# Optimization experiments

Measured on AMD Instinct MI355X. Metric: run time of the kernel, lower is better.

The kernel has to match this reference:

```python
import jax, jax.numpy as jnp
import numpy as np

B, N, D_IN, D_HID, D_OUT = 64, 512, 512, 512, 512


def setup_inputs() -> dict:
    key = jax.random.key(0)
    ks = jax.random.split(key, 8)
    gain = 0.02  # xavier_normal_ gain used in reset_parameters_xavier

    def xavier(k, fan_in, fan_out):
        std = gain * np.sqrt(2.0 / (fan_in + fan_out))
        return jax.random.normal(k, (fan_in, fan_out), dtype=jnp.float32) * std

    return {
        "batch_graph": jax.random.normal(ks[0], (B, N, D_IN), dtype=jnp.float32),
        "adj": jax.random.uniform(ks[1], (B, N, N), dtype=jnp.float32),
        "W1": xavier(ks[2], D_IN, D_HID),
        "b1": jnp.zeros((D_HID,), dtype=jnp.float32),
        "W2": xavier(ks[3], D_HID, D_HID),
        "b2": jnp.zeros((D_HID,), dtype=jnp.float32),
        "W3": xavier(ks[4], D_HID, D_OUT),
        "b3": jnp.zeros((D_OUT,), dtype=jnp.float32),
    }


def _normalize_adj(adj):
    # rowsum^-0.5 with inf -> 0 (original: torch.pow then isinf mask)
    rowsum = adj.sum(axis=1)                       # [B, N] (sum over dim 1, as in torch)
    safe = jnp.where(rowsum == 0, 1.0, rowsum)
    r = jnp.where(rowsum == 0, 0.0, safe ** -0.5)  # [B, N]
    # (adj @ D)^T @ D = D @ adj^T @ D with D = diag(r)
    return r[:, :, None] * jnp.swapaxes(adj, 1, 2) * r[:, None, :]


def reference(batch_graph, adj, W1, b1, W2, b2, W3, b3):
    # Block-diagonal big_adj @ big_graph == per-graph batched matmul.
    A = _normalize_adj(adj)  # [B, N, N]

    def gc(x, W, b):
        # support = x @ W ; output = A @ support + b
        return jnp.einsum('bij,bjd->bid', A, x @ W) + b

    # dropout is identity in eval mode (deterministic reference)
    x = jax.nn.relu(gc(batch_graph, W1, b1))
    x = jax.nn.relu(gc(x, W2, b2))
    return gc(x, W3, b3)  # [B, N, D_OUT]
```

## Files before the change

kernel.cpp:

```cpp
#include <hip/hip_runtime.h>
#include <cstdint>
#include <cstddef>

typedef _Float16 f16;
typedef _Float16 f16x4 __attribute__((ext_vector_type(4)));
typedef _Float16 f16x8 __attribute__((ext_vector_type(8)));
typedef float    f32x4 __attribute__((ext_vector_type(4)));

#define NB 64
#define NN 262144

__device__ __forceinline__ void gload_lds16(const void* g, void* l) {
    __builtin_amdgcn_global_load_lds(
        (const __attribute__((address_space(1))) void*)g,
        (__attribute__((address_space(3))) void*)l, 16, 0, 0);
}

__device__ __forceinline__ int SWC(int row, int col) {
    return ((((col >> 2) ^ (row >> 2)) & 15) << 2) | (col & 3);
}

__global__ __launch_bounds__(256)
void k_prep(const float* __restrict__ adj, f16* __restrict__ A_raw,
            float* __restrict__ part,
            const float* __restrict__ W1, const float* __restrict__ W2,
            const float* __restrict__ W3, f16* __restrict__ Wt,
            const float* __restrict__ X0, f16* __restrict__ Xa) {
    __shared__ __align__(16) float t[4096];
    __shared__ float red[4][64];
    const int bid = blockIdx.x, tid = threadIdx.x;

    bool do_cvt = false;
    int cvt_idx = 0;
    if (bid < 8192) {
        if (bid & 1) { do_cvt = true; cvt_idx = bid >> 1; }
    } else if (bid < 12288) {
        do_cvt = true; cvt_idx = 4096 + (bid - 8192);
    }

    if (do_cvt) {
        size_t i = ((size_t)cvt_idx * 256 + tid) * 8;
        float4 v0 = *(const float4*)(X0 + i);
        float4 v1 = *(const float4*)(X0 + i + 4);
        f16x8 o;
        o[0] = (f16)v0.x; o[1] = (f16)v0.y; o[2] = (f16)v0.z; o[3] = (f16)v0.w;
        o[4] = (f16)v1.x; o[5] = (f16)v1.y; o[6] = (f16)v1.z; o[7] = (f16)v1.w;
        *(f16x8*)(Xa + i) = o;
    } else if (bid < 8192) {
        const int idx = bid >> 1;
        const int xcd = idx & 7, loc = idx >> 3;
        const int b = xcd * 8 + (loc >> 6);
        const int tile = loc & 63;
        const int i0 = (tile >> 3) * 64, j0 = (tile & 7) * 64;
        const int jt = tile & 7;
        const float* ab = adj + (size_t)b * NN;
        #pragma unroll
        for (int s = 0; s < 4; ++s) {
            int rr = s * 16 + (tid >> 4);
            int creal = SWC(rr, (tid & 15) * 4);
            gload_lds16(&ab[(size_t)(j0 + rr) * 512 + i0 + creal],
                        &t[s * 1024 + tid * 4]);
        }
        asm volatile("s_waitcnt vmcnt(0)" ::: "memory");
        __syncthreads();
        {
            int c = tid & 63, g = tid >> 6;
            float sg = 0.f;
            #pragma unroll
            for (int s = 0; s < 16; ++s) {
                int row = g * 16 + s;
                sg += t[row * 64 + SWC(row, c)];
            }
            red[g][c] = sg;
        }
        f16* Ab = A_raw + (size_t)b * NN;
        int jq = (tid & 15) * 4;
        int ib = tid >> 4;
        #pragma unroll
        for (int s = 0; s < 4; ++s) {
            int ii = ib + s * 16;
            f16x4 o;
            #pragma unroll
            for (int q = 0; q < 4; ++q)
                o[q] = (f16)t[(jq + q) * 64 + SWC(jq + q, ii)];
            *(f16x4*)&Ab[(size_t)(i0 + ii) * 512 + j0 + jq] = o;
        }
        __syncthreads();
        if (tid < 64)
            part[((size_t)b * 8 + jt) * 512 + i0 + tid] =
                red[0][tid] + red[1][tid] + red[2][tid] + red[3][tid];
    } else {
        int cb = bid - 12288;
        int z = cb >> 6, rem = cb & 63;
        const float* W = z == 0 ? W1 : (z == 1 ? W2 : W3);
        f16* out = Wt + (size_t)z * NN;
        int k0 = (rem >> 3) * 64, d0 = (rem & 7) * 64;
        int c = tid & 63, r4 = tid >> 6;
        #pragma unroll
        for (int s = 0; s < 16; ++s) {
            int rr = r4 + s * 4;
            t[rr * 64 + SWC(rr, c)] = W[(size_t)(k0 + rr) * 512 + d0 + c];
        }
        __syncthreads();
        int kq = (tid & 15) * 4;
        int db = tid >> 4;
        #pragma unroll
        for (int s = 0; s < 4; ++s) {
            int dd = db + s * 16;
            f16x4 o;
            #pragma unroll
            for (int q = 0; q < 4; ++q)
                o[q] = (f16)(64.f * t[(kq + q) * 64 + SWC(kq + q, dd)]);
            *(f16x4*)&out[(size_t)(d0 + dd) * 512 + k0 + kq] = o;
        }
    }
}

template<bool BIAS, bool RELU, bool OUTF32, bool RM, bool RN>
__global__ __launch_bounds__(512, 1)
void gemm8(const f16* __restrict__ P, size_t pstr,
           const f16* __restrict__ Qt, size_t qstr,
           void* __restrict__ Cout, size_t cstr,
           const float* __restrict__ bias, const float* __restrict__ part,
           float iscale, float oscale) {
    __shared__ __align__(16) f16 Albuf[2][16384];
    __shared__ __align__(16) f16 Blbuf[2][16384];
    __shared__ float rs_lds[256];

    const int tid  = threadIdx.x;
    const int lane = tid & 63;
    const int wid  = tid >> 6;
    const int wm   = wid >> 2;
    const int wn   = wid & 3;

    const int wg  = blockIdx.x;
    const int swz = (wg & 7) * 32 + (wg >> 3);
    const int b   = swz >> 2;
    const int tt  = swz & 3;
    const int m0  = (tt >> 1) * 256;
    const int n0  = (tt & 1) * 256;

    const f16* Pb = P + (size_t)b * pstr;
    const f16* Qb = Qt + (size_t)b * qstr;

    const int fr = lane & 15, fs = lane >> 4, fx = fr & 7;

    if ((RM || RN) && tid < 256) {
        const float* p = part + (size_t)b * 4096 + (RM ? m0 : n0) + tid;
        float s = 0.f;
        #pragma unroll
        for (int jt = 0; jt < 8; ++jt) s += p[jt * 512];
        rs_lds[tid] = (s > 0.f) ? rsqrtf(s) : 0.f;
    }
    asm volatile("s_waitcnt vmcnt(0)" ::: "memory");

    auto stage_half = [&](const f16* __restrict__ Gb, int row0g, f16* buf, int h, int k0) {
        {
            int row = tid >> 3, sl = tid & 7;
            gload_lds16(Gb + (size_t)(row0g + h * 128 + row) * 512 + k0 + ((sl ^ (row & 7)) * 8),
                        buf + h * 8192 + tid * 8);
        }
        {
            int u = tid + 512;
            int row = u >> 3, sl = u & 7;
            gload_lds16(Gb + (size_t)(row0g + h * 128 + row) * 512 + k0 + ((sl ^ (row & 7)) * 8),
                        buf + h * 8192 + u * 8);
        }
    };

    f32x4 acc[8][4] = {};
    f16x8 af[4][2], bf[2][2];

    stage_half(Qb, n0, &Blbuf[0][0], 0, 0);
    stage_half(Qb, n0, &Blbuf[0][0], 1, 0);
    stage_half(Pb, m0, &Albuf[0][0], 0, 0);
    stage_half(Pb, m0, &Albuf[0][0], 1, 0);

#define LOAD_AF(QM)                                                            \
    _Pragma("unroll") for (int i = 0; i < 4; ++i) {                            \
        int row = wm * 128 + ((QM) * 4 + i) * 16 + fr;                         \
        _Pragma("unroll") for (int k = 0; k < 2; ++k)                          \
            af[i][k] = *(const f16x8*)&Al[row * 64 + ((fs + 4 * k) ^ fx) * 8]; \
    }
#define LOAD_BF(QN)                                                            \
    _Pragma("unroll") for (int j = 0; j < 2; ++j) {                            \
        int row = wn * 64 + ((QN) * 2 + j) * 16 + fr;                          \
        _Pragma("unroll") for (int k = 0; k < 2; ++k)                          \
            bf[j][k] = *(const f16x8*)&Bl[row * 64 + ((fs + 4 * k) ^ fx) * 8]; \
    }
#define PH_SYNC()                                                              \
    __builtin_amdgcn_s_barrier();                                              \
    asm volatile("s_waitcnt lgkmcnt(0)" ::: "memory");                         \
    __builtin_amdgcn_sched_barrier(0);
#define DO_MFMA(QM, QN)                                                        \
    __builtin_amdgcn_s_setprio(1);                                             \
    _Pragma("unroll") for (int i = 0; i < 4; ++i)                              \
        _Pragma("unroll") for (int j = 0; j < 2; ++j)                          \
            _Pragma("unroll") for (int k = 0; k < 2; ++k)                      \
                acc[(QM) * 4 + i][(QN) * 2 + j] =                              \
                    __builtin_amdgcn_mfma_f32_16x16x32_f16(                    \
                        af[i][k], bf[j][k], acc[(QM) * 4 + i][(QN) * 2 + j],   \
                        0, 0, 0);                                              \
    __builtin_amdgcn_s_setprio(0);                                             \
    __builtin_amdgcn_s_barrier();

    for (int t = 0; t < 8; ++t) {
        f16* Al = &Albuf[t & 1][0];
        f16* Bl = &Blbuf[t & 1][0];
        f16* An = &Albuf[(t & 1) ^ 1][0];
        f16* Bn = &Blbuf[(t & 1) ^ 1][0];
        const int kn = (t + 1) * 64;

        asm volatile("s_waitcnt vmcnt(0)" ::: "memory");
        __builtin_amdgcn_s_barrier();

        LOAD_AF(0) LOAD_BF(0)
        if (t < 7) stage_half(Qb, n0, Bn, 0, kn);
        PH_SYNC(); DO_MFMA(0, 0)
        LOAD_BF(1)
        if (t < 7) stage_half(Qb, n0, Bn, 1, kn);
        PH_SYNC(); DO_MFMA(0, 1)
        LOAD_AF(1)
        if (t < 7) stage_half(Pb, m0, An, 0, kn);
        PH_SYNC(); DO_MFMA(1, 1)
        LOAD_BF(0)
        if (t < 7) stage_half(Pb, m0, An, 1, kn);
        PH_SYNC(); DO_MFMA(1, 0)
    }
#undef LOAD_AF
#undef LOAD_BF
#undef PH_SYNC
#undef DO_MFMA

    const int cmb = (lane >> 4) * 4;
    f32x4 rm4[8];
    float rn1[4];
    if (RM) {
        #pragma unroll
        for (int mi = 0; mi < 8; ++mi)
            rm4[mi] = *(const f32x4*)&rs_lds[wm * 128 + mi * 16 + cmb];
    }
    if (RN) {
        #pragma unroll
        for (int ni = 0; ni < 4; ++ni)
            rn1[ni] = rs_lds[wn * 64 + ni * 16 + fr];
    }
    #pragma unroll
    for (int mi = 0; mi < 8; ++mi) {
        #pragma unroll
        for (int ni = 0; ni < 4; ++ni) {
            const int n = n0 + wn * 64 + ni * 16 + fr;
            const int m = m0 + wm * 128 + mi * 16 + cmb;
            float v[4];
            #pragma unroll
            for (int q = 0; q < 4; ++q) {
                float x = acc[mi][ni][q] * iscale;
                if (RM) x *= rm4[mi][q];
                if (RN) x *= rn1[ni];
                if (BIAS) x += bias[m + q];
                if (RELU) x = fmaxf(x, 0.f);
                v[q] = x * oscale;
            }
            if (OUTF32) {
                float* Cb = (float*)Cout + (size_t)b * cstr;
                f32x4 o; o[0] = v[0]; o[1] = v[1]; o[2] = v[2]; o[3] = v[3];
                *(f32x4*)&Cb[(size_t)n * 512 + m] = o;
            } else {
                f16* Cb = (f16*)Cout + (size_t)b * cstr;
                f16x4 o; o[0] = (f16)v[0]; o[1] = (f16)v[1]; o[2] = (f16)v[2]; o[3] = (f16)v[3];
                *(f16x4*)&Cb[(size_t)n * 512 + m] = o;
            }
        }
    }
}

extern "C" void kernel_launch(void* const* d_in, const int* in_sizes, int n_in,
                              void* d_out, int out_size, void* d_ws, size_t ws_size,
                              hipStream_t stream) {
    const float* X0  = (const float*)d_in[0];
    const float* adj = (const float*)d_in[1];
    const float* W1  = (const float*)d_in[2];
    const float* b1  = (const float*)d_in[3];
    const float* W2  = (const float*)d_in[4];
    const float* b2  = (const float*)d_in[5];
    const float* W3  = (const float*)d_in[6];
    const float* b3  = (const float*)d_in[7];

    uint8_t* ws = (uint8_t*)d_ws;
    float* part = (float*)ws;
    f16* Wt1 = (f16*)(ws + (1 << 20));
    f16* A_raw = (f16*)(ws + (1 << 20) + (size_t)3 * NN * 2);
    f16* Xa  = A_raw + (size_t)NB * NN;
    f16* S_t = Xa + (size_t)NB * NN;

    k_prep<<<dim3(12480), dim3(256), 0, stream>>>(adj, A_raw, part, W1, W2, W3, Wt1, X0, Xa);

    dim3 gg(256), gb(512);
    gemm8<false, false, false, true,  false><<<gg, gb, 0, stream>>>(Xa,  (size_t)NN, Wt1, (size_t)0,  S_t, (size_t)NN, nullptr, part, 4.f, 1.f);
    gemm8<true,  true,  false, false, true ><<<gg, gb, 0, stream>>>(S_t, (size_t)NN, A_raw, (size_t)NN, Xa, (size_t)NN, b1, part, 1.f / 256.f, 256.f);
    gemm8<false, false, false, true,  false><<<gg, gb, 0, stream>>>(Xa,  (size_t)NN, Wt1 + NN, (size_t)0,  S_t, (size_t)NN, nullptr, part, 16.f, 1.f);
    gemm8<true,  true,  false, false, true ><<<gg, gb, 0, stream>>>(S_t, (size_t)NN, A_raw, (size_t)NN, Xa, (size_t)NN, b2, part, 1.f / 262144.f, 256.f);
    gemm8<false, false, false, true,  false><<<gg, gb, 0, stream>>>(Xa,  (size_t)NN, Wt1 + 2 * NN, (size_t)0,  S_t, (size_t)NN, nullptr, part, 16.f, 1.f);
    gemm8<true,  false, true,  false, true ><<<gg, gb, 0, stream>>>(S_t, (size_t)NN, A_raw, (size_t)NN, d_out, (size_t)NN, b3, part, 1.f / 262144.f, 1.f);
}
```

Measured before the change: 200.9 us.

## Make prep kernel persistent with double-buffered async LDS staging

The prep kernel's grid shrinks from thousands of single-tile blocks to about 2k blocks. Each block loops over several conversion chunks or transpose tiles and prefetches the next chunk into a second LDS buffer while processing the current one. X conversion now also goes through LDS via async global-to-LDS loads, and the W transpose shares the adj tile path with a scale factor. The intent is to hide memory latency and cut block launch overhead. The risk is fewer resident waves for latency hiding and extra barriers per iteration.

```diff
diff --git a/kernel.cpp b/kernel.cpp
--- a/kernel.cpp
+++ b/kernel.cpp
@@ -26,44 +26,92 @@
             const float* __restrict__ W1, const float* __restrict__ W2,
             const float* __restrict__ W3, f16* __restrict__ Wt,
             const float* __restrict__ X0, f16* __restrict__ Xa) {
-    __shared__ __align__(16) float t[4096];
+    __shared__ __align__(16) float tb[2][4096];
     __shared__ float red[4][64];
     const int bid = blockIdx.x, tid = threadIdx.x;
 
-    bool do_cvt = false;
-    int cvt_idx = 0;
-    if (bid < 8192) {
-        if (bid & 1) { do_cvt = true; cvt_idx = bid >> 1; }
-    } else if (bid < 12288) {
-        do_cvt = true; cvt_idx = 4096 + (bid - 8192);
-    }
-
-    if (do_cvt) {
-        size_t i = ((size_t)cvt_idx * 256 + tid) * 8;
-        float4 v0 = *(const float4*)(X0 + i);
-        float4 v1 = *(const float4*)(X0 + i + 4);
-        f16x8 o;
-        o[0] = (f16)v0.x; o[1] = (f16)v0.y; o[2] = (f16)v0.z; o[3] = (f16)v0.w;
-        o[4] = (f16)v1.x; o[5] = (f16)v1.y; o[6] = (f16)v1.z; o[7] = (f16)v1.w;
-        *(f16x8*)(Xa + i) = o;
-    } else if (bid < 8192) {
-        const int idx = bid >> 1;
-        const int xcd = idx & 7, loc = idx >> 3;
-        const int b = xcd * 8 + (loc >> 6);
-        const int tile = loc & 63;
-        const int i0 = (tile >> 3) * 64, j0 = (tile & 7) * 64;
-        const int jt = tile & 7;
-        const float* ab = adj + (size_t)b * NN;
+    const bool is_cvt = (bid < 2048) && (bid & 1);
+    if (is_cvt) {
+        const int cw = bid >> 1;
+        auto stage_u = [&](int k, int buf) {
+            const float* src = X0 + (size_t)(cw * 8 + k) * 2048;
+            gload_lds16(src + tid * 4,          &tb[buf][tid * 4]);
+            gload_lds16(src + (tid + 256) * 4,  &tb[buf][(tid + 256) * 4]);
+        };
+        stage_u(0, 0);
+        #pragma unroll 1
+        for (int k = 0; k < 8; ++k) {
+            const int buf = k & 1;
+            if (k < 7) {
+                stage_u(k + 1, buf ^ 1);
+                asm volatile("s_waitcnt vmcnt(2)" ::: "memory");
+            } else {
+                asm volatile("s_waitcnt vmcnt(0)" ::: "memory");
+            }
+            __builtin_amdgcn_s_barrier();
+            f32x4 v0 = *(const f32x4*)&tb[buf][tid * 8];
+            f32x4 v1 = *(const f32x4*)&tb[buf][tid * 8 + 4];
+            f16x8 o;
+            o[0] = (f16)v0[0]; o[1] = (f16)v0[1]; o[2] = (f16)v0[2]; o[3] = (f16)v0[3];
+            o[4] = (f16)v1[0]; o[5] = (f16)v1[1]; o[6] = (f16)v1[2]; o[7] = (f16)v1[3];
+            *(f16x8*)(Xa + (size_t)(cw * 8 + k) * 2048 + tid * 8) = o;
+            asm volatile("s_waitcnt lgkmcnt(0)" ::: "memory");
+            __builtin_amdgcn_s_barrier();
+        }
+        return;
+    }
+
+    const int tw = (bid < 2048) ? (bid >> 1) : (bid - 1024);
+    auto decode = [&](int jj, const float*& src, f16*& dst, float& scale,
+                      float*& pp) {
+        int job = tw * 4 + jj;
+        if (job < 4096) {
+            int xcd = job & 7, loc = job >> 3;
+            int b = xcd * 8 + (loc >> 6);
+            int tile = loc & 63;
+            int i0 = (tile >> 3) * 64, j0 = (tile & 7) * 64;
+            src = adj + (size_t)b * NN + (size_t)j0 * 512 + i0;
+            dst = A_raw + (size_t)b * NN + (size_t)i0 * 512 + j0;
+            scale = 1.f;
+            pp = part + ((size_t)b * 8 + (tile & 7)) * 512 + i0;
+        } else {
+            int w = job - 4096;
+            int z = w >> 6, rem = w & 63;
+            int k0 = (rem >> 3) * 64, d0 = (rem & 7) * 64;
+            const float* W = z == 0 ? W1 : (z == 1 ? W2 : W3);
+            src = W + (size_t)k0 * 512 + d0;
+            dst = Wt + (size_t)z * NN + (size_t)d0 * 512 + k0;
+            scale = 64.f;
+            pp = nullptr;
+        }
+    };
+    auto stage_j = [&](int jj, int buf) {
+        const float* src; f16* dst; float sc; float* pp;
+        decode(jj, src, dst, sc, pp);
         #pragma unroll
         for (int s = 0; s < 4; ++s) {
             int rr = s * 16 + (tid >> 4);
             int creal = SWC(rr, (tid & 15) * 4);
-            gload_lds16(&ab[(size_t)(j0 + rr) * 512 + i0 + creal],
-                        &t[s * 1024 + tid * 4]);
-        }
-        asm volatile("s_waitcnt vmcnt(0)" ::: "memory");
-        __syncthreads();
-        {
+            gload_lds16(src + (size_t)rr * 512 + creal, &tb[buf][s * 1024 + tid * 4]);
+        }
+    };
+
+    stage_j(0, 0);
+    #pragma unroll 1
+    for (int jj = 0; jj < 4; ++jj) {
+        const int buf = jj & 1;
+        if (jj < 3) {
+            stage_j(jj + 1, buf ^ 1);
+            asm volatile("s_waitcnt vmcnt(4)" ::: "memory");
+        } else {
+            asm volatile("s_waitcnt vmcnt(0)" ::: "memory");
+        }
+        __builtin_amdgcn_s_barrier();
+
+        const float* src; f16* dst; float sc; float* pp;
+        decode(jj, src, dst, sc, pp);
+        const float* t = &tb[buf][0];
+        if (pp) {
             int c = tid & 63, g = tid >> 6;
             float sg = 0.f;
             #pragma unroll
@@ -73,46 +121,24 @@
             }
             red[g][c] = sg;
         }
-        f16* Ab = A_raw + (size_t)b * NN;
-        int jq = (tid & 15) * 4;
-        int ib = tid >> 4;
-        #pragma unroll
-        for (int s = 0; s < 4; ++s) {
-            int ii = ib + s * 16;
-            f16x4 o;
+        {
+            int jq = (tid & 15) * 4;
+            int ib = tid >> 4;
             #pragma unroll
-            for (int q = 0; q < 4; ++q)
-                o[q] = (f16)t[(jq + q) * 64 + SWC(jq + q, ii)];
-            *(f16x4*)&Ab[(size_t)(i0 + ii) * 512 + j0 + jq] = o;
-        }
-        __syncthreads();
-        if (tid < 64)
-            part[((size_t)b * 8 + jt) * 512 + i0 + tid] =
-                red[0][tid] + red[1][tid] + red[2][tid] + red[3][tid];
-    } else {
-        int cb = bid - 12288;
-        int z = cb >> 6, rem = cb & 63;
-        const float* W = z == 0 ? W1 : (z == 1 ? W2 : W3);
-        f16* out = Wt + (size_t)z * NN;
-        int k0 = (rem >> 3) * 64, d0 = (rem & 7) * 64;
-        int c = tid & 63, r4 = tid >> 6;
-        #pragma unroll
-        for (int s = 0; s < 16; ++s) {
-            int rr = r4 + s * 4;
-            t[rr * 64 + SWC(rr, c)] = W[(size_t)(k0 + rr) * 512 + d0 + c];
-        }
-        __syncthreads();
-        int kq = (tid & 15) * 4;
-        int db = tid >> 4;
-        #pragma unroll
-        for (int s = 0; s < 4; ++s) {
-            int dd = db + s * 16;
-            f16x4 o;
-            #pragma unroll
-            for (int q = 0; q < 4; ++q)
-                o[q] = (f16)(64.f * t[(kq + q) * 64 + SWC(kq + q, dd)]);
-            *(f16x4*)&out[(size_t)(d0 + dd) * 512 + k0 + kq] = o;
-        }
+            for (int s = 0; s < 4; ++s) {
+                int ii = ib + s * 16;
+                f16x4 o;
+                #pragma unroll
+                for (int q = 0; q < 4; ++q)
+                    o[q] = (f16)(sc * t[(jq + q) * 64 + SWC(jq + q, ii)]);
+                *(f16x4*)&dst[(size_t)ii * 512 + jq] = o;
+            }
+        }
+        asm volatile("s_waitcnt lgkmcnt(0)" ::: "memory");
+        __builtin_amdgcn_s_barrier();
+        if (pp && tid < 64)
+            pp[tid] = red[0][tid] + red[1][tid] + red[2][tid] + red[3][tid];
+        __builtin_amdgcn_s_barrier();
     }
 }
 
@@ -293,7 +319,7 @@
     f16* Xa  = A_raw + (size_t)NB * NN;
     f16* S_t = Xa + (size_t)NB * NN;
 
-    k_prep<<<dim3(12480), dim3(256), 0, stream>>>(adj, A_raw, part, W1, W2, W3, Wt1, X0, Xa);
+    k_prep<<<dim3(2096), dim3(256), 0, stream>>>(adj, A_raw, part, W1, W2, W3, Wt1, X0, Xa);
 
     dim3 gg(256), gb(512);
     gemm8<false, false, false, true,  false><<<gg, gb, 0, stream>>>(Xa,  (size_t)NN, Wt1, (size_t)0,  S_t, (size_t)NN, nullptr, part, 4.f, 1.f);
```

Result: slower. 215.7 us (+7.4%).
